# Kernel tuning notes

Hardware: AMD Instinct MI355X
Metric: run time of the kernel (lower is better)

Reference implementation:

```python
import jax, jax.numpy as jnp
import numpy as np

N, IN_DIM, HID, E, NUM_TASKS, TED = 8192, 1024, 2048, 4, 8, 100
MU = 0.01
EPS = 1e-6


def setup_inputs() -> dict:
    key = jax.random.key(0)
    ks = jax.random.split(key, 8)
    s_in = 1.0 / np.sqrt(IN_DIM)
    s_h = 1.0 / np.sqrt(HID)
    return {
        "backbone_output": jax.random.normal(ks[0], (N, IN_DIM), dtype=jnp.float32),
        "task": jax.random.randint(ks[1], (N,), 0, NUM_TASKS),
        "task_embeddings": jax.random.normal(ks[2], (NUM_TASKS, TED), dtype=jnp.float32),
        "routing_matrix": jax.random.normal(ks[3], (IN_DIM + TED, E), dtype=jnp.float32) * 0.05,
        "W1": jax.random.uniform(ks[4], (E, IN_DIM, HID), jnp.float32, -s_in, s_in),
        "b1": jax.random.uniform(ks[5], (E, HID), jnp.float32, -s_in, s_in),
        "W2": jax.random.uniform(ks[6], (E, HID, HID), jnp.float32, -s_h, s_h),
        "b2": jax.random.uniform(ks[7], (E, HID), jnp.float32, -s_h, s_h),
    }


def _gram_schmidt(x):
    # x: [N, E, H] -> orthonormal basis along expert axis via sequential GS
    b0 = x[:, 0] / jnp.linalg.norm(x[:, 0], axis=-1, keepdims=True)
    basis = [b0]
    for i in range(1, x.shape[1]):
        v = x[:, i]                           # [N, H]
        B = jnp.stack(basis, axis=1)          # [N, i, H]
        coef = jnp.einsum("nh,nih->ni", v, B)
        w = v - jnp.einsum("ni,nih->nh", coef, B)
        basis.append(w / jnp.linalg.norm(w, axis=-1, keepdims=True))
    return jnp.stack(basis, axis=1)           # [N, E, H]


def reference(backbone_output, task, task_embeddings, routing_matrix, W1, b1, W2, b2):
    # router: softmax over experts on [x ; task_emb[task]] @ R
    router_in = jnp.concatenate([backbone_output, task_embeddings[task]], axis=-1)
    weights = jax.nn.softmax(router_in @ routing_matrix, axis=-1)   # [N, E]

    # per-expert 2-layer ReLU MLP, all experts at once
    h = jax.nn.relu(jnp.einsum("ni,eih->neh", backbone_output, W1) + b1[None])
    expert_outputs = jax.nn.relu(jnp.einsum("neh,ehk->nek", h, W2) + b2[None])  # [N,E,H]

    # top-1 gate: keep only max weight, zero the rest
    idx = jnp.argmax(weights, axis=-1)
    gates = jnp.where(jnp.arange(weights.shape[-1])[None, :] == idx[:, None], weights, 0.0)

    ortho = _gram_schmidt(expert_outputs)
    tower_input = jnp.einsum("ne,neh->nh", gates, ortho)

    reg_loss = -(1.0 / E) * MU * jnp.sum(jnp.log(gates + EPS), axis=-1)
    return tower_input, reg_loss
```

## Files before the change

kernel.cpp:

```cpp
#include <hip/hip_runtime.h>
#include <hip/hip_bf16.h>
#include <cstdint>

#define N_SAMP 8192
#define IN_DIM 1024
#define HID    2048
#define NE     4

typedef __attribute__((ext_vector_type(8))) __bf16 bf16x8;
typedef __attribute__((ext_vector_type(4))) float  f32x4;

#define MFMA16 __builtin_amdgcn_mfma_f32_16x16x32_bf16

__device__ __forceinline__ unsigned short f2b(float f) {
    unsigned u = __float_as_uint(f);
    u += 0x7fff + ((u >> 16) & 1);
    return (unsigned short)(u >> 16);
}
__device__ __forceinline__ float b2f(unsigned short s) {
    return __uint_as_float(((unsigned)s) << 16);
}

__device__ __forceinline__ void gll16(const void* g, void* l) {
    __builtin_amdgcn_global_load_lds(
        (const __attribute__((address_space(1))) void*)g,
        (__attribute__((address_space(3))) void*)l,
        16, 0, 0);
}

__device__ __forceinline__ int swz(int byte) {
    return byte ^ (((byte >> 7) & 7) << 4);
}

__global__ void conv_bf16(const float* __restrict__ s, unsigned short* __restrict__ d, int n) {
    int i = (blockIdx.x * blockDim.x + threadIdx.x) * 4;
    if (i >= n) return;
    float4 v = *(const float4*)&s[i];
    ushort4 o;
    o.x = f2b(v.x); o.y = f2b(v.y); o.z = f2b(v.z); o.w = f2b(v.w);
    *(ushort4*)&d[i] = o;
}

__global__ void transpose_conv(const float* __restrict__ src, unsigned short* __restrict__ dst,
                               int K, int M) {
    __shared__ float tile[64][65];
    const int k0 = blockIdx.x * 64, m0 = blockIdx.y * 64;
    const int t  = threadIdx.x;
    const int tc = t & 15, tr = t >> 4;
    const float* s = src + (size_t)k0 * M + m0;
    #pragma unroll
    for (int r = tr; r < 64; r += 16) {
        float4 v = *(const float4*)&s[(size_t)r * M + tc * 4];
        tile[r][tc * 4 + 0] = v.x; tile[r][tc * 4 + 1] = v.y;
        tile[r][tc * 4 + 2] = v.z; tile[r][tc * 4 + 3] = v.w;
    }
    __syncthreads();
    unsigned short* d = dst + (size_t)m0 * K + k0;
    #pragma unroll
    for (int r = tr; r < 64; r += 16) {
        ushort4 o;
        o.x = f2b(tile[tc * 4 + 0][r]); o.y = f2b(tile[tc * 4 + 1][r]);
        o.z = f2b(tile[tc * 4 + 2][r]); o.w = f2b(tile[tc * 4 + 3][r]);
        *(ushort4*)&d[(size_t)r * K + tc * 4] = o;
    }
}

__global__ void router_kernel(const float* __restrict__ bb, const int* __restrict__ task,
                              const float* __restrict__ temb, const float* __restrict__ rm,
                              float* __restrict__ gval, int* __restrict__ gidx,
                              float* __restrict__ regout) {
    const int t = threadIdx.x, wave = t >> 6, lane = t & 63;
    const int n = blockIdx.x * 4 + wave;
    const int tk = task[n];
    float a0 = 0.f, a1 = 0.f, a2 = 0.f, a3 = 0.f;
    for (int i = lane; i < IN_DIM + 100; i += 64) {
        float x = (i < IN_DIM) ? bb[(size_t)n * IN_DIM + i] : temb[tk * 100 + (i - IN_DIM)];
        float4 r = *(const float4*)&rm[i * 4];
        a0 += x * r.x; a1 += x * r.y; a2 += x * r.z; a3 += x * r.w;
    }
    #pragma unroll
    for (int o = 32; o; o >>= 1) {
        a0 += __shfl_xor(a0, o); a1 += __shfl_xor(a1, o);
        a2 += __shfl_xor(a2, o); a3 += __shfl_xor(a3, o);
    }
    if (lane == 0) {
        float l[4] = {a0, a1, a2, a3};
        float mx = fmaxf(fmaxf(l[0], l[1]), fmaxf(l[2], l[3]));
        float ex[4], s = 0.f;
        #pragma unroll
        for (int j = 0; j < 4; j++) { ex[j] = expf(l[j] - mx); s += ex[j]; }
        int bi = 0; float bw = ex[0];
        #pragma unroll
        for (int j = 1; j < 4; j++) if (ex[j] > bw) { bw = ex[j]; bi = j; }
        float g = bw / s;
        gval[n] = g;
        gidx[n] = bi;
        regout[n] = -0.0025f * (logf(g + 1e-6f) + 3.0f * logf(1e-6f));
    }
}

__global__ void compact_kernel(const int* __restrict__ gidx, int* __restrict__ list,
                               int* __restrict__ pos, int* __restrict__ cnt) {
    const int e = blockIdx.x;
    const int t = threadIdx.x, lane = t & 63, wave = t >> 6;
    __shared__ int wbase[4];
    __shared__ int running;
    if (t == 0) running = 0;
    __syncthreads();
    int* le = list + (size_t)e * N_SAMP;
    int* pe = pos + (size_t)e * N_SAMP;
    for (int base = 0; base < N_SAMP; base += 256) {
        const int n = base + t;
        const bool f = gidx[n] >= e;
        unsigned long long m = __ballot(f);
        int rank = __popcll(m & ((1ULL << lane) - 1ULL));
        if (lane == 0) wbase[wave] = __popcll(m);
        __syncthreads();
        int wb = 0;
        #pragma unroll
        for (int w = 0; w < 4; w++) if (w < wave) wb += wbase[w];
        int tot = wbase[0] + wbase[1] + wbase[2] + wbase[3];
        int o = running + wb + rank;
        if (f) { le[o] = n; pe[n] = o; }
        __syncthreads();
        if (t == 0) running += tot;
        __syncthreads();
    }
    const int c = running;
    if (t == 0) cnt[e] = c;
    const int padded = (c + 255) & ~255;
    for (int i = c + t; i < padded && i < N_SAMP; i += 256) le[i] = 0;
}

template<int KT>
__device__ __forceinline__ void gemm_core(
    const unsigned short* __restrict__ A, const unsigned short* __restrict__ BT,
    const float* __restrict__ bias, unsigned short* __restrict__ C,
    int M, const int* __restrict__ rowlist, const int* __restrict__ cntp,
    int bid, char* lds_) {
    constexpr int nt = KT / 64;
    const int cnt = *cntp;
    const int mb = bid & 7, nb = bid >> 3;
    const int n0 = nb * 256;
    if (n0 >= cnt) return;
    const int m0 = mb * 256;
    const int t = threadIdx.x;
    const int w = t >> 6, lane = t & 63;
    const int wm = w >> 2, wn = w & 3;
    const int lrow = lane & 15, kg = lane >> 4;

    int rr[2], cb[2];
    #pragma unroll
    for (int q = 0; q < 2; q++) {
        int Ps = swz((t + q * 512) * 16);
        rr[q] = Ps >> 7;
        cb[q] = Ps & 127;
    }
    const char* aS[2][2];
    const char* bS[2][2];
    #pragma unroll
    for (int h = 0; h < 2; h++)
        #pragma unroll
        for (int q = 0; q < 2; q++) {
            int r = n0 + h * 128 + rr[q];
            int ga = rowlist ? rowlist[r] : r;
            aS[h][q] = (const char*)A + (size_t)ga * (KT * 2) + cb[q];
            bS[h][q] = (const char*)BT + (size_t)(m0 + h * 128 + rr[q]) * (KT * 2) + cb[q];
        }

    auto stageA = [&](int buf, int h, int kt) {
        gll16(aS[h][0] + kt * 128, lds_ + buf * 65536 + h * 16384 + w * 1024);
        gll16(aS[h][1] + kt * 128, lds_ + buf * 65536 + h * 16384 + 8192 + w * 1024);
    };
    auto stageB = [&](int buf, int h, int kt) {
        gll16(bS[h][0] + kt * 128, lds_ + buf * 65536 + 32768 + h * 16384 + w * 1024);
        gll16(bS[h][1] + kt * 128, lds_ + buf * 65536 + 32768 + h * 16384 + 8192 + w * 1024);
    };

    const int mask = (lrow & 7) << 4;
    const int c0 = (kg * 16) ^ mask;
    const int c1 = (kg * 16 + 64) ^ mask;
    const char* const pA[2] = { lds_ + wm * 16384 + lrow * 128 + c0,
                                lds_ + wm * 16384 + lrow * 128 + c1 };
    const int browB = (wn & 1) * 64 + lrow;
    const char* const pB[2] = { lds_ + 32768 + (wn >> 1) * 16384 + browB * 128 + c0,
                                lds_ + 32768 + (wn >> 1) * 16384 + browB * 128 + c1 };
    auto ldA = [&](int buf, int i, int kk) -> bf16x8 {
        return *(const bf16x8*)(pA[kk] + buf * 65536 + i * 2048);
    };
    auto ldB = [&](int buf, int j, int kk) -> bf16x8 {
        return *(const bf16x8*)(pB[kk] + buf * 65536 + j * 2048);
    };

    f32x4 acc[8][4];
    #pragma unroll
    for (int i = 0; i < 8; i++)
        #pragma unroll
        for (int j = 0; j < 4; j++) acc[i][j] = (f32x4){0.f, 0.f, 0.f, 0.f};

    stageA(0, 0, 0); stageA(0, 1, 0); stageB(0, 0, 0); stageB(0, 1, 0);
    stageA(1, 0, 1); stageA(1, 1, 1); stageB(1, 0, 1);
    asm volatile("s_waitcnt vmcnt(6)" ::: "memory");
    __builtin_amdgcn_s_barrier();

    bf16x8 af[4][2], bfr[4][2];
    auto tile = [&](int kt, int buf) {
        #pragma unroll
        for (int i = 0; i < 4; i++) { af[i][0] = ldA(buf, i, 0); af[i][1] = ldA(buf, i, 1); }
        #pragma unroll
        for (int j = 0; j < 2; j++) { bfr[j][0] = ldB(buf, j, 0); bfr[j][1] = ldB(buf, j, 1); }
        if (kt + 1 < nt) stageB(buf ^ 1, 1, kt + 1);
        __builtin_amdgcn_s_barrier();
        __builtin_amdgcn_s_setprio(1);
        #pragma unroll
        for (int i = 0; i < 4; i++)
            #pragma unroll
            for (int j = 0; j < 2; j++) {
                acc[i][j] = MFMA16(af[i][0], bfr[j][0], acc[i][j], 0, 0, 0);
                acc[i][j] = MFMA16(af[i][1], bfr[j][1], acc[i][j], 0, 0, 0);
            }
        __builtin_amdgcn_s_setprio(0);
        __builtin_amdgcn_s_barrier();
        #pragma unroll
        for (int j = 2; j < 4; j++) { bfr[j][0] = ldB(buf, j, 0); bfr[j][1] = ldB(buf, j, 1); }
        __builtin_amdgcn_s_barrier();
        __builtin_amdgcn_s_setprio(1);
        #pragma unroll
        for (int i = 0; i < 4; i++)
            #pragma unroll
            for (int j = 0; j < 2; j++) {
                acc[i][2 + j] = MFMA16(af[i][0], bfr[2 + j][0], acc[i][2 + j], 0, 0, 0);
                acc[i][2 + j] = MFMA16(af[i][1], bfr[2 + j][1], acc[i][2 + j], 0, 0, 0);
            }
        __builtin_amdgcn_s_setprio(0);
        __builtin_amdgcn_s_barrier();
        #pragma unroll
        for (int i = 0; i < 4; i++) { af[i][0] = ldA(buf, 4 + i, 0); af[i][1] = ldA(buf, 4 + i, 1); }
        if (kt + 2 < nt) stageB(buf, 0, kt + 2);
        __builtin_amdgcn_s_barrier();
        __builtin_amdgcn_s_setprio(1);
        #pragma unroll
        for (int i = 0; i < 4; i++)
            #pragma unroll
            for (int j = 0; j < 2; j++) {
                acc[4 + i][j] = MFMA16(af[i][0], bfr[j][0], acc[4 + i][j], 0, 0, 0);
                acc[4 + i][j] = MFMA16(af[i][1], bfr[j][1], acc[4 + i][j], 0, 0, 0);
            }
        __builtin_amdgcn_s_setprio(0);
        __builtin_amdgcn_s_barrier();
        if (kt + 2 < nt) { stageA(buf, 0, kt + 2); stageA(buf, 1, kt + 2); }
        __builtin_amdgcn_s_barrier();
        __builtin_amdgcn_s_setprio(1);
        #pragma unroll
        for (int i = 0; i < 4; i++)
            #pragma unroll
            for (int j = 0; j < 2; j++) {
                acc[4 + i][2 + j] = MFMA16(af[i][0], bfr[2 + j][0], acc[4 + i][2 + j], 0, 0, 0);
                acc[4 + i][2 + j] = MFMA16(af[i][1], bfr[2 + j][1], acc[4 + i][2 + j], 0, 0, 0);
            }
        __builtin_amdgcn_s_setprio(0);
        if (kt < nt - 2) asm volatile("s_waitcnt vmcnt(6)" ::: "memory");
        else             asm volatile("s_waitcnt vmcnt(0)" ::: "memory");
        __builtin_amdgcn_s_barrier();
    };
    for (int kt = 0; kt < nt; kt += 2) { tile(kt, 0); tile(kt + 1, 1); }

    float bv[4];
    #pragma unroll
    for (int j = 0; j < 4; j++)
        bv[j] = bias[m0 + wn * 64 + j * 16 + lrow];
    #pragma unroll
    for (int i = 0; i < 8; i++) {
        const int srow0 = n0 + wm * 128 + i * 16 + kg * 4;
        #pragma unroll
        for (int j = 0; j < 4; j++) {
            const int col = m0 + wn * 64 + j * 16 + lrow;
            #pragma unroll
            for (int q = 0; q < 4; q++) {
                if (srow0 + q < cnt) {
                    float x = acc[i][j][q] + bv[j];
                    C[(size_t)(srow0 + q) * M + col] = f2b(fmaxf(x, 0.f));
                }
            }
        }
    }
}

template<int KT>
__global__ __launch_bounds__(512, 2) void gemm256(
    const unsigned short* __restrict__ A, const unsigned short* __restrict__ BT,
    const float* __restrict__ bias, unsigned short* __restrict__ C,
    int M, const int* __restrict__ rowlist, const int* __restrict__ cntp) {
    extern __shared__ char lds_[];
    gemm_core<KT>(A, BT, bias, C, M, rowlist, cntp, blockIdx.x, lds_);
}

__global__ __launch_bounds__(512, 2) void gemm256_dual(
    const unsigned short* __restrict__ A2, const unsigned short* __restrict__ BT2,
    const float* __restrict__ bias2, unsigned short* __restrict__ C2,
    const int* __restrict__ cnt2,
    const unsigned short* __restrict__ A1, const unsigned short* __restrict__ BT1,
    const float* __restrict__ bias1, unsigned short* __restrict__ C1,
    const int* __restrict__ rowlist1, const int* __restrict__ cnt1) {
    extern __shared__ char lds_[];
    const int bid = blockIdx.x;
    if (bid < 256) {
        gemm_core<HID>(A2, BT2, bias2, C2, HID, nullptr, cnt2, bid, lds_);
    } else {
        gemm_core<IN_DIM>(A1, BT1, bias1, C1, HID, rowlist1, cnt1, bid - 256, lds_);
    }
}

__global__ void gs_kernel(const unsigned short* __restrict__ eo, const float* __restrict__ gval,
                          const int* __restrict__ gidx, const int* __restrict__ pos,
                          float* __restrict__ dout) {
    const int t = threadIdx.x, wave = t >> 6, lane = t & 63;
    const int n = blockIdx.x * 4 + wave;
    const int idx = gidx[n];
    const float g = gval[n];

    float v[32], b0[32], b1[32], b2[32];

    auto loadv = [&](float* dst, int e) {
        const size_t row = pos[(size_t)e * N_SAMP + n];
        const unsigned short* p = eo + ((size_t)e * N_SAMP + row) * HID + lane * 8;
        #pragma unroll
        for (int c = 0; c < 4; c++) {
            uint4 u = *(const uint4*)(p + c * 512);
            const unsigned short* us = (const unsigned short*)&u;
            #pragma unroll
            for (int j = 0; j < 8; j++) dst[c * 8 + j] = b2f(us[j]);
        }
    };
    auto wdot = [&](const float* x, const float* y) -> float {
        float s = 0.f;
        #pragma unroll
        for (int k = 0; k < 32; k++) s += x[k] * y[k];
        #pragma unroll
        for (int o = 32; o; o >>= 1) s += __shfl_xor(s, o);
        return s;
    };
    auto storev = [&](const float* b) {
        float* o = dout + (size_t)n * HID + lane * 8;
        #pragma unroll
        for (int c = 0; c < 4; c++) {
            float4 x0, x1;
            x0.x = g * b[c * 8 + 0]; x0.y = g * b[c * 8 + 1];
            x0.z = g * b[c * 8 + 2]; x0.w = g * b[c * 8 + 3];
            x1.x = g * b[c * 8 + 4]; x1.y = g * b[c * 8 + 5];
            x1.z = g * b[c * 8 + 6]; x1.w = g * b[c * 8 + 7];
            *(float4*)(o + c * 512) = x0;
            *(float4*)(o + c * 512 + 4) = x1;
        }
    };

    loadv(v, 0);
    float inv = 1.f / sqrtf(wdot(v, v));
    #pragma unroll
    for (int k = 0; k < 32; k++) b0[k] = v[k] * inv;
    if (idx == 0) { storev(b0); return; }
    loadv(v, 1);
    {
        float cc0 = wdot(v, b0);
        #pragma unroll
        for (int k = 0; k < 32; k++) v[k] -= cc0 * b0[k];
        inv = 1.f / sqrtf(wdot(v, v));
        #pragma unroll
        for (int k = 0; k < 32; k++) b1[k] = v[k] * inv;
    }
    if (idx == 1) { storev(b1); return; }
    loadv(v, 2);
    {
        float cc0 = wdot(v, b0);
        float cc1 = wdot(v, b1);
        #pragma unroll
        for (int k = 0; k < 32; k++) v[k] -= cc0 * b0[k] + cc1 * b1[k];
        inv = 1.f / sqrtf(wdot(v, v));
        #pragma unroll
        for (int k = 0; k < 32; k++) b2[k] = v[k] * inv;
    }
    if (idx == 2) { storev(b2); return; }
    loadv(v, 3);
    {
        float cc0 = wdot(v, b0);
        float cc1 = wdot(v, b1);
        float cc2 = wdot(v, b2);
        #pragma unroll
        for (int k = 0; k < 32; k++) v[k] -= cc0 * b0[k] + cc1 * b1[k] + cc2 * b2[k];
        inv = 1.f / sqrtf(wdot(v, v));
        #pragma unroll
        for (int k = 0; k < 32; k++) v[k] *= inv;
    }
    storev(v);
}

extern "C" void kernel_launch(void* const* d_in, const int* in_sizes, int n_in,
                              void* d_out, int out_size, void* d_ws, size_t ws_size,
                              hipStream_t stream) {
    const float* bb   = (const float*)d_in[0];
    const int*   task = (const int*)d_in[1];
    const float* temb = (const float*)d_in[2];
    const float* rm   = (const float*)d_in[3];
    const float* W1   = (const float*)d_in[4];
    const float* b1   = (const float*)d_in[5];
    const float* W2   = (const float*)d_in[6];
    const float* b2   = (const float*)d_in[7];
    float* out = (float*)d_out;

    char* ws = (char*)d_ws;
    unsigned short* obf  = (unsigned short*)(ws + 0);
    unsigned short* Abf  = (unsigned short*)(ws + 134217728);
    unsigned short* hbfA = (unsigned short*)(ws + 150994944);
    unsigned short* W1T  = (unsigned short*)(ws + 184549376);
    unsigned short* W2T  = (unsigned short*)(ws + 188743680);
    float*          gv   = (float*)(ws + 197132288);
    int*            gi   = (int*)(ws + 197165056);
    int*            list = (int*)(ws + 197197824);
    int*            pos  = (int*)(ws + 197328896);
    int*            cnt  = (int*)(ws + 197459968);
    unsigned short* hbfB = obf + (size_t)3 * N_SAMP * HID;
    auto hbf = [&](int e) { return (e & 1) ? hbfA : hbfB; };

    conv_bf16<<<(N_SAMP * IN_DIM) / 1024, 256, 0, stream>>>(bb, Abf, N_SAMP * IN_DIM);
    router_kernel<<<N_SAMP / 4, 256, 0, stream>>>(bb, task, temb, rm, gv, gi,
                                                  out + (size_t)N_SAMP * HID);
    compact_kernel<<<NE, 256, 0, stream>>>(gi, list, pos, cnt);

    const size_t lds_bytes = 131072;

    transpose_conv<<<dim3(IN_DIM / 64, HID / 64), 256, 0, stream>>>(W1, W1T, IN_DIM, HID);
    gemm256<IN_DIM><<<256, 512, lds_bytes, stream>>>(
        Abf, W1T, b1, hbf(0), HID, list, cnt);

    for (int e = 0; e < 3; ++e) {
        transpose_conv<<<dim3(HID / 64, HID / 64), 256, 0, stream>>>(
            W2 + (size_t)e * HID * HID, W2T, HID, HID);
        transpose_conv<<<dim3(IN_DIM / 64, HID / 64), 256, 0, stream>>>(
            W1 + (size_t)(e + 1) * IN_DIM * HID, W1T, IN_DIM, HID);
        gemm256_dual<<<512, 512, lds_bytes, stream>>>(
            hbf(e), W2T, b2 + (size_t)e * HID, obf + (size_t)e * N_SAMP * HID, cnt + e,
            Abf, W1T, b1 + (size_t)(e + 1) * HID, hbf(e + 1),
            list + (size_t)(e + 1) * N_SAMP, cnt + e + 1);
    }

    transpose_conv<<<dim3(HID / 64, HID / 64), 256, 0, stream>>>(
        W2 + (size_t)3 * HID * HID, W2T, HID, HID);
    gemm256<HID><<<256, 512, lds_bytes, stream>>>(
        hbf(3), W2T, b2 + (size_t)3 * HID, obf + (size_t)3 * N_SAMP * HID, HID,
        nullptr, cnt + 3);

    gs_kernel<<<N_SAMP / 4, 256, 0, stream>>>(obf, gv, gi, pos, out);
}
```

Measured before the change: 544.0 us.

## Reschedule expert GEMMs into paired dual launches with separate buffers

When the workspace is large enough, each expert gets its own hidden buffer and weight-transpose buffers are doubled. The schedule then becomes four dual-GEMM launches instead of single GEMMs at the start and end: layer-1 for experts 0 and 1 together, two mixed layer-1/layer-2 launches, and layer-2 for experts 2 and 3 together. The aim is to avoid the half-occupied 256-block launches at the edges of the pipeline. It needs about 46 MB more workspace and keeps the old schedule as a fallback, so whether the new path runs depends on the workspace size the harness provides.

```diff
diff --git a/kernel.cpp b/kernel.cpp
--- a/kernel.cpp
+++ b/kernel.cpp
@@ -311,6 +311,35 @@
     }
 }
 
+__global__ __launch_bounds__(512, 2) void gemm256_dual_g1g1(
+    const unsigned short* __restrict__ A,
+    const unsigned short* __restrict__ BTa, const float* __restrict__ biasa,
+    unsigned short* __restrict__ Ca, const int* __restrict__ rla, const int* __restrict__ cnta,
+    const unsigned short* __restrict__ BTb, const float* __restrict__ biasb,
+    unsigned short* __restrict__ Cb, const int* __restrict__ rlb, const int* __restrict__ cntb) {
+    extern __shared__ char lds_[];
+    const int bid = blockIdx.x;
+    if (bid < 256) {
+        gemm_core<IN_DIM>(A, BTa, biasa, Ca, HID, rla, cnta, bid, lds_);
+    } else {
+        gemm_core<IN_DIM>(A, BTb, biasb, Cb, HID, rlb, cntb, bid - 256, lds_);
+    }
+}
+
+__global__ __launch_bounds__(512, 2) void gemm256_dual_g2g2(
+    const unsigned short* __restrict__ Aa, const unsigned short* __restrict__ BTa,
+    const float* __restrict__ biasa, unsigned short* __restrict__ Ca, const int* __restrict__ cnta,
+    const unsigned short* __restrict__ Ab, const unsigned short* __restrict__ BTb,
+    const float* __restrict__ biasb, unsigned short* __restrict__ Cb, const int* __restrict__ cntb) {
+    extern __shared__ char lds_[];
+    const int bid = blockIdx.x;
+    if (bid < 256) {
+        gemm_core<HID>(Aa, BTa, biasa, Ca, HID, nullptr, cnta, bid, lds_);
+    } else {
+        gemm_core<HID>(Ab, BTb, biasb, Cb, HID, nullptr, cntb, bid - 256, lds_);
+    }
+}
+
 __global__ void gs_kernel(const unsigned short* __restrict__ eo, const float* __restrict__ gval,
                           const int* __restrict__ gidx, const int* __restrict__ pos,
                           float* __restrict__ dout) {
@@ -406,48 +435,104 @@
     const float* W2   = (const float*)d_in[6];
     const float* b2   = (const float*)d_in[7];
     float* out = (float*)d_out;
-
     char* ws = (char*)d_ws;
-    unsigned short* obf  = (unsigned short*)(ws + 0);
-    unsigned short* Abf  = (unsigned short*)(ws + 134217728);
-    unsigned short* hbfA = (unsigned short*)(ws + 150994944);
-    unsigned short* W1T  = (unsigned short*)(ws + 184549376);
-    unsigned short* W2T  = (unsigned short*)(ws + 188743680);
-    float*          gv   = (float*)(ws + 197132288);
-    int*            gi   = (int*)(ws + 197165056);
-    int*            list = (int*)(ws + 197197824);
-    int*            pos  = (int*)(ws + 197328896);
-    int*            cnt  = (int*)(ws + 197459968);
-    unsigned short* hbfB = obf + (size_t)3 * N_SAMP * HID;
-    auto hbf = [&](int e) { return (e & 1) ? hbfA : hbfB; };
-
-    conv_bf16<<<(N_SAMP * IN_DIM) / 1024, 256, 0, stream>>>(bb, Abf, N_SAMP * IN_DIM);
-    router_kernel<<<N_SAMP / 4, 256, 0, stream>>>(bb, task, temb, rm, gv, gi,
-                                                  out + (size_t)N_SAMP * HID);
-    compact_kernel<<<NE, 256, 0, stream>>>(gi, list, pos, cnt);
 
     const size_t lds_bytes = 131072;
-
-    transpose_conv<<<dim3(IN_DIM / 64, HID / 64), 256, 0, stream>>>(W1, W1T, IN_DIM, HID);
-    gemm256<IN_DIM><<<256, 512, lds_bytes, stream>>>(
-        Abf, W1T, b1, hbf(0), HID, list, cnt);
-
-    for (int e = 0; e < 3; ++e) {
+    const size_t PLAN_A_NEED = 243597376;
+
+    if (ws_size >= PLAN_A_NEED) {
+        unsigned short* obf  = (unsigned short*)(ws + 0);
+        unsigned short* h0   = (unsigned short*)(ws + 33554432);
+        unsigned short* h1   = (unsigned short*)(ws + 67108864);
+        unsigned short* Abf  = (unsigned short*)(ws + 134217728);
+        unsigned short* h2   = (unsigned short*)(ws + 150994944);
+        unsigned short* h3   = (unsigned short*)(ws + 184549376);
+        unsigned short* W1Ta = (unsigned short*)(ws + 218103808);
+        unsigned short* W1Tb = (unsigned short*)(ws + 222298112);
+        unsigned short* W2Ta = (unsigned short*)(ws + 226492416);
+        unsigned short* W2Tb = (unsigned short*)(ws + 234881024);
+        float*          gv   = (float*)(ws + 243269632);
+        int*            gi   = (int*)(ws + 243302400);
+        int*            list = (int*)(ws + 243335168);
+        int*            pos  = (int*)(ws + 243466240);
+        int*            cnt  = (int*)(ws + 243597312);
+
+        conv_bf16<<<(N_SAMP * IN_DIM) / 1024, 256, 0, stream>>>(bb, Abf, N_SAMP * IN_DIM);
+        router_kernel<<<N_SAMP / 4, 256, 0, stream>>>(bb, task, temb, rm, gv, gi,
+                                                      out + (size_t)N_SAMP * HID);
+        compact_kernel<<<NE, 256, 0, stream>>>(gi, list, pos, cnt);
+
+        transpose_conv<<<dim3(IN_DIM / 64, HID / 64), 256, 0, stream>>>(W1, W1Ta, IN_DIM, HID);
+        transpose_conv<<<dim3(IN_DIM / 64, HID / 64), 256, 0, stream>>>(
+            W1 + (size_t)1 * IN_DIM * HID, W1Tb, IN_DIM, HID);
+        gemm256_dual_g1g1<<<512, 512, lds_bytes, stream>>>(
+            Abf, W1Ta, b1, h0, list, cnt,
+            W1Tb, b1 + HID, h1, list + N_SAMP, cnt + 1);
+
+        transpose_conv<<<dim3(HID / 64, HID / 64), 256, 0, stream>>>(W2, W2Ta, HID, HID);
+        transpose_conv<<<dim3(IN_DIM / 64, HID / 64), 256, 0, stream>>>(
+            W1 + (size_t)2 * IN_DIM * HID, W1Ta, IN_DIM, HID);
+        gemm256_dual<<<512, 512, lds_bytes, stream>>>(
+            h0, W2Ta, b2, obf, cnt,
+            Abf, W1Ta, b1 + 2 * HID, h2, list + (size_t)2 * N_SAMP, cnt + 2);
+
         transpose_conv<<<dim3(HID / 64, HID / 64), 256, 0, stream>>>(
-            W2 + (size_t)e * HID * HID, W2T, HID, HID);
+            W2 + (size_t)1 * HID * HID, W2Tb, HID, HID);
         transpose_conv<<<dim3(IN_DIM / 64, HID / 64), 256, 0, stream>>>(
-            W1 + (size_t)(e + 1) * IN_DIM * HID, W1T, IN_DIM, HID);
+            W1 + (size_t)3 * IN_DIM * HID, W1Tb, IN_DIM, HID);
         gemm256_dual<<<512, 512, lds_bytes, stream>>>(
-            hbf(e), W2T, b2 + (size_t)e * HID, obf + (size_t)e * N_SAMP * HID, cnt + e,
-            Abf, W1T, b1 + (size_t)(e + 1) * HID, hbf(e + 1),
-            list + (size_t)(e + 1) * N_SAMP, cnt + e + 1);
-    }
-
-    transpose_conv<<<dim3(HID / 64, HID / 64), 256, 0, stream>>>(
-        W2 + (size_t)3 * HID * HID, W2T, HID, HID);
-    gemm256<HID><<<256, 512, lds_bytes, stream>>>(
-        hbf(3), W2T, b2 + (size_t)3 * HID, obf + (size_t)3 * N_SAMP * HID, HID,
-        nullptr, cnt + 3);
-
-    gs_kernel<<<N_SAMP / 4, 256, 0, stream>>>(obf, gv, gi, pos, out);
-}
+            h1, W2Tb, b2 + HID, obf + (size_t)1 * N_SAMP * HID, cnt + 1,
+            Abf, W1Tb, b1 + 3 * HID, h3, list + (size_t)3 * N_SAMP, cnt + 3);
+
+        transpose_conv<<<dim3(HID / 64, HID / 64), 256, 0, stream>>>(
+            W2 + (size_t)2 * HID * HID, W2Ta, HID, HID);
+        transpose_conv<<<dim3(HID / 64, HID / 64), 256, 0, stream>>>(
+            W2 + (size_t)3 * HID * HID, W2Tb, HID, HID);
+        gemm256_dual_g2g2<<<512, 512, lds_bytes, stream>>>(
+            h2, W2Ta, b2 + 2 * HID, obf + (size_t)2 * N_SAMP * HID, cnt + 2,
+            h3, W2Tb, b2 + 3 * HID, obf + (size_t)3 * N_SAMP * HID, cnt + 3);
+
+        gs_kernel<<<N_SAMP / 4, 256, 0, stream>>>(obf, gv, gi, pos, out);
+    } else {
+        unsigned short* obf  = (unsigned short*)(ws + 0);
+        unsigned short* Abf  = (unsigned short*)(ws + 134217728);
+        unsigned short* hbfA = (unsigned short*)(ws + 150994944);
+        unsigned short* W1T  = (unsigned short*)(ws + 184549376);
+        unsigned short* W2T  = (unsigned short*)(ws + 188743680);
+        float*          gv   = (float*)(ws + 197132288);
+        int*            gi   = (int*)(ws + 197165056);
+        int*            list = (int*)(ws + 197197824);
+        int*            pos  = (int*)(ws + 197328896);
+        int*            cnt  = (int*)(ws + 197459968);
+        unsigned short* hbfB = obf + (size_t)3 * N_SAMP * HID;
+        auto hbf = [&](int e) { return (e & 1) ? hbfA : hbfB; };
+
+        conv_bf16<<<(N_SAMP * IN_DIM) / 1024, 256, 0, stream>>>(bb, Abf, N_SAMP * IN_DIM);
+        router_kernel<<<N_SAMP / 4, 256, 0, stream>>>(bb, task, temb, rm, gv, gi,
+                                                      out + (size_t)N_SAMP * HID);
+        compact_kernel<<<NE, 256, 0, stream>>>(gi, list, pos, cnt);
+
+        transpose_conv<<<dim3(IN_DIM / 64, HID / 64), 256, 0, stream>>>(W1, W1T, IN_DIM, HID);
+        gemm256<IN_DIM><<<256, 512, lds_bytes, stream>>>(
+            Abf, W1T, b1, hbf(0), HID, list, cnt);
+
+        for (int e = 0; e < 3; ++e) {
+            transpose_conv<<<dim3(HID / 64, HID / 64), 256, 0, stream>>>(
+                W2 + (size_t)e * HID * HID, W2T, HID, HID);
+            transpose_conv<<<dim3(IN_DIM / 64, HID / 64), 256, 0, stream>>>(
+                W1 + (size_t)(e + 1) * IN_DIM * HID, W1T, IN_DIM, HID);
+            gemm256_dual<<<512, 512, lds_bytes, stream>>>(
+                hbf(e), W2T, b2 + (size_t)e * HID, obf + (size_t)e * N_SAMP * HID, cnt + e,
+                Abf, W1T, b1 + (size_t)(e + 1) * HID, hbf(e + 1),
+                list + (size_t)(e + 1) * N_SAMP, cnt + e + 1);
+        }
+
+        transpose_conv<<<dim3(HID / 64, HID / 64), 256, 0, stream>>>(
+            W2 + (size_t)3 * HID * HID, W2T, HID, HID);
+        gemm256<HID><<<256, 512, lds_bytes, stream>>>(
+            hbf(3), W2T, b2 + (size_t)3 * HID, obf + (size_t)3 * N_SAMP * HID, HID,
+            nullptr, cnt + 3);
+
+        gs_kernel<<<N_SAMP / 4, 256, 0, stream>>>(obf, gv, gi, pos, out);
+    }
+}
```

Result: faster. 497.8 us (-8.5%).
